# Performance work log

Measured on AMD Instinct MI355X. Metric: run time of the kernel, lower is better.

## Reference

```python
import jax, jax.numpy as jnp
import numpy as np

ALPHA = 0.2  # LeakyReLU negative slope

def setup_inputs() -> dict:
    key = jax.random.key(0)
    k1, k2, k3, k4 = jax.random.split(key, 4)
    B, N, IN_C, OUT_C = 4, 4096, 64, 64
    features = jax.random.normal(k1, (B, N, IN_C), dtype=jnp.float32)
    adj = jax.random.uniform(k2, (B, N, N), dtype=jnp.float32)  # unused by the module's math
    # xavier_normal approximations
    W = jax.random.normal(k3, (IN_C, OUT_C), dtype=jnp.float32) * np.sqrt(2.0 / (IN_C + OUT_C))
    a = jax.random.normal(k4, (2 * OUT_C, 1), dtype=jnp.float32) * np.sqrt(2.0 / (2 * OUT_C + 1))
    return {"features": features, "adj": adj, "W": W, "a": a}

def reference(features, adj, W, a):
    # h: [B, N, F]
    h = jnp.matmul(features, W)
    out_c = W.shape[1]
    a1 = a[:out_c, 0]   # [F]
    a2 = a[out_c:, 0]   # [F]
    # e[b,i,j] = leakyrelu(h_i . a1 + h_j . a2)  (decomposed; avoids O(N^2*2F) concat)
    s1 = jnp.einsum('bnf,f->bn', h, a1)  # [B, N]
    s2 = jnp.einsum('bnf,f->bn', h, a2)  # [B, N]
    e = s1[:, :, None] + s2[:, None, :]  # [B, N, N]
    e = jnp.where(e >= 0, e, ALPHA * e)  # leaky relu
    attention = jax.nn.softmax(e, axis=2)  # note: adj is NOT used (faithful to source)
    h_prime = jnp.matmul(attention, h)  # [B, N, F]
    return h_prime
```

## Files before the change

kernel.cpp:

```cpp
#include <hip/hip_runtime.h>
#include <hip/hip_bf16.h>
#include <cmath>

#define LRALPHA 0.2f

namespace {
constexpr int BB = 4;
constexpr int NN = 4096;
constexpr int ROWS = BB * NN;
}

typedef __attribute__((ext_vector_type(8))) short bf16x8;
typedef __attribute__((ext_vector_type(4))) float f32x4;

static __device__ inline short f2bf(float x) {
  __hip_bfloat16 t = __float2bfloat16(x);
  return *reinterpret_cast<short*>(&t);
}
static __device__ inline float bf2f(short x) {
  __hip_bfloat16 t = *reinterpret_cast<__hip_bfloat16*>(&x);
  return __bfloat162float(t);
}
static __device__ inline unsigned int packRNE(float a, float b) {
  unsigned int ua = __float_as_uint(a), ub = __float_as_uint(b);
  unsigned int ra = ua + 0x7FFFu + ((ua >> 16) & 1u);
  unsigned int rb = ub + 0x7FFFu + ((ub >> 16) & 1u);
  return (ra >> 16) | (rb & 0xFFFF0000u);
}

__global__ __launch_bounds__(256) void k_hcvt(
    const float* __restrict__ feat, const float* __restrict__ W,
    const float* __restrict__ a,
    unsigned short* __restrict__ hTh, unsigned short* __restrict__ hTl,
    float* __restrict__ s1g, float* __restrict__ s2g) {
  __shared__ float tile[64][65];
  const int lane = threadIdx.x & 63;
  const int wave = threadIdx.x >> 6;
  const int row0 = blockIdx.x * 64;

  float wreg[64];
#pragma unroll
  for (int k = 0; k < 64; ++k) wreg[k] = W[k * 64 + lane];
  const float a1 = a[lane], a2 = a[64 + lane];

  for (int r = 0; r < 16; ++r) {
    const int row = row0 + wave * 16 + r;
    const float4* f4 = (const float4*)(feat + (size_t)row * 64);
    float hv = 0.f;
#pragma unroll
    for (int kk = 0; kk < 16; ++kk) {
      float4 f = f4[kk];
      hv = fmaf(f.x, wreg[4 * kk + 0], hv);
      hv = fmaf(f.y, wreg[4 * kk + 1], hv);
      hv = fmaf(f.z, wreg[4 * kk + 2], hv);
      hv = fmaf(f.w, wreg[4 * kk + 3], hv);
    }
    tile[wave * 16 + r][lane] = hv;
    float p1 = hv * a1, p2 = hv * a2;
#pragma unroll
    for (int off = 32; off; off >>= 1) {
      p1 += __shfl_xor(p1, off, 64);
      p2 += __shfl_xor(p2, off, 64);
    }
    if (lane == 0) { s1g[row] = p1; s2g[row] = p2; }
  }
  __syncthreads();

  const int b = row0 >> 12;
  const int n0 = row0 & (NN - 1);
#pragma unroll
  for (int cc = 0; cc < 16; ++cc) {
    int ch = cc * 4 + wave;
    float v = tile[lane][ch];
    short hi = f2bf(v);
    short lo = f2bf(v - bf2f(hi));
    size_t idx = ((size_t)(b * 64 + ch) << 12) + n0 + lane;
    hTh[idx] = (unsigned short)hi;
    hTl[idx] = (unsigned short)lo;
  }
}

__global__ void k_maxs2(const float* __restrict__ s2g, float* __restrict__ maxs2) {
  __shared__ float red[256];
  int b = blockIdx.x;
  float m = -1e30f;
  for (int j = threadIdx.x; j < NN; j += 256) m = fmaxf(m, s2g[b * NN + j]);
  red[threadIdx.x] = m;
  __syncthreads();
  for (int off = 128; off; off >>= 1) {
    if ((int)threadIdx.x < off) red[threadIdx.x] = fmaxf(red[threadIdx.x], red[threadIdx.x + off]);
    __syncthreads();
  }
  if (threadIdx.x == 0) maxs2[b] = red[0];
}

__global__ void k_prep(const float* __restrict__ s1g, const float* __restrict__ s2g,
                       const float* __restrict__ maxs2,
                       float* __restrict__ Ag, float* __restrict__ Apg,
                       float* __restrict__ Tg,
                       float* __restrict__ Bv, float* __restrict__ Bpv) {
  int row = blockIdx.x * 256 + threadIdx.x;
  int b = row >> 12;
  float s1 = s1g[row], s2 = s2g[row];
  float t = s1 + maxs2[b];
  float m = t >= 0.f ? t : LRALPHA * t;
  Ag[row]  = expf(s1 - m);
  Apg[row] = expf(LRALPHA * s1 - m);
  Tg[row]  = expf(-s1);
  Bv[row]  = expf(s2);
  Bpv[row] = expf(LRALPHA * s2);
}

__global__ __launch_bounds__(512, 4) void k_attn(
    const unsigned short* __restrict__ hTh, const unsigned short* __restrict__ hTl,
    const float* __restrict__ Ag, const float* __restrict__ Apg,
    const float* __restrict__ Tg,
    const float* __restrict__ Bv, const float* __restrict__ Bpv,
    float* __restrict__ out) {
  __shared__ float slab[4][32][65];
  __shared__ float l_lds[4][32];

  const int wave = threadIdx.x >> 6;
  const int lane = threadIdx.x & 63;
  const int m = lane & 15;
  const int quad = lane >> 4;
  const int row0 = blockIdx.x * 32;
  const int b = row0 >> 12;
  const int i0 = row0 + m, i1 = row0 + 16 + m;

  const float Ar0 = Ag[i0], Ap0 = Apg[i0], T0 = Tg[i0];
  const float Ar1 = Ag[i1], Ap1 = Apg[i1], T1 = Tg[i1];

  f32x4 acc00 = {0,0,0,0}, acc01 = {0,0,0,0}, acc02 = {0,0,0,0}, acc03 = {0,0,0,0};
  f32x4 acc10 = {0,0,0,0}, acc11 = {0,0,0,0}, acc12 = {0,0,0,0}, acc13 = {0,0,0,0};
  f32x4 lacc0 = {0,0,0,0}, lacc1 = {0,0,0,0};

  bf16x8 ones;
#pragma unroll
  for (int e = 0; e < 8; ++e) ones[e] = (short)0x3F80;

  const int j0 = wave * (NN / 8) + quad * 8;
  const float* Bq  = Bv  + (b << 12) + j0;
  const float* Bpq = Bpv + (b << 12) + j0;
  const unsigned short* hp = hTh + ((size_t)(b * 64 + m) << 12) + j0;
  const unsigned short* lp = hTl + ((size_t)(b * 64 + m) << 12) + j0;
  constexpr size_t CH16 = (size_t)16 << 12;

  for (int it = 0; it < NN / 8 / 32; ++it) {
    float4 bA = *(const float4*)(Bq);
    float4 bB = *(const float4*)(Bq + 4);
    float4 pA = *(const float4*)(Bpq);
    float4 pB = *(const float4*)(Bpq + 4);
    float bvv[8] = {bA.x, bA.y, bA.z, bA.w, bB.x, bB.y, bB.z, bB.w};
    float pvv[8] = {pA.x, pA.y, pA.z, pA.w, pB.x, pB.y, pB.z, pB.w};

    float w0v[8], w1v[8];
#pragma unroll
    for (int e = 0; e < 8; ++e) {
      float Bj = bvv[e], Bpj = pvv[e];
      w0v[e] = (Bj >= T0) ? (Ar0 * Bj) : (Ap0 * Bpj);
      w1v[e] = (Bj >= T1) ? (Ar1 * Bj) : (Ap1 * Bpj);
    }
    union { bf16x8 v; unsigned int u[4]; } af0u, af1u;
#pragma unroll
    for (int p = 0; p < 4; ++p) {
      af0u.u[p] = packRNE(w0v[2 * p], w0v[2 * p + 1]);
      af1u.u[p] = packRNE(w1v[2 * p], w1v[2 * p + 1]);
    }
    bf16x8 af0 = af0u.v, af1 = af1u.v;

    bf16x8 hh0 = *(const bf16x8*)(hp);
    bf16x8 hh1 = *(const bf16x8*)(hp + CH16);
    bf16x8 hh2 = *(const bf16x8*)(hp + 2 * CH16);
    bf16x8 hh3 = *(const bf16x8*)(hp + 3 * CH16);
    bf16x8 hl0 = *(const bf16x8*)(lp);
    bf16x8 hl1 = *(const bf16x8*)(lp + CH16);
    bf16x8 hl2 = *(const bf16x8*)(lp + 2 * CH16);
    bf16x8 hl3 = *(const bf16x8*)(lp + 3 * CH16);

    lacc0 = __builtin_amdgcn_mfma_f32_16x16x32_bf16(af0, ones, lacc0, 0, 0, 0);
    lacc1 = __builtin_amdgcn_mfma_f32_16x16x32_bf16(af1, ones, lacc1, 0, 0, 0);
    acc00 = __builtin_amdgcn_mfma_f32_16x16x32_bf16(af0, hh0, acc00, 0, 0, 0);
    acc00 = __builtin_amdgcn_mfma_f32_16x16x32_bf16(af0, hl0, acc00, 0, 0, 0);
    acc01 = __builtin_amdgcn_mfma_f32_16x16x32_bf16(af0, hh1, acc01, 0, 0, 0);
    acc01 = __builtin_amdgcn_mfma_f32_16x16x32_bf16(af0, hl1, acc01, 0, 0, 0);
    acc02 = __builtin_amdgcn_mfma_f32_16x16x32_bf16(af0, hh2, acc02, 0, 0, 0);
    acc02 = __builtin_amdgcn_mfma_f32_16x16x32_bf16(af0, hl2, acc02, 0, 0, 0);
    acc03 = __builtin_amdgcn_mfma_f32_16x16x32_bf16(af0, hh3, acc03, 0, 0, 0);
    acc03 = __builtin_amdgcn_mfma_f32_16x16x32_bf16(af0, hl3, acc03, 0, 0, 0);
    acc10 = __builtin_amdgcn_mfma_f32_16x16x32_bf16(af1, hh0, acc10, 0, 0, 0);
    acc10 = __builtin_amdgcn_mfma_f32_16x16x32_bf16(af1, hl0, acc10, 0, 0, 0);
    acc11 = __builtin_amdgcn_mfma_f32_16x16x32_bf16(af1, hh1, acc11, 0, 0, 0);
    acc11 = __builtin_amdgcn_mfma_f32_16x16x32_bf16(af1, hl1, acc11, 0, 0, 0);
    acc12 = __builtin_amdgcn_mfma_f32_16x16x32_bf16(af1, hh2, acc12, 0, 0, 0);
    acc12 = __builtin_amdgcn_mfma_f32_16x16x32_bf16(af1, hl2, acc12, 0, 0, 0);
    acc13 = __builtin_amdgcn_mfma_f32_16x16x32_bf16(af1, hh3, acc13, 0, 0, 0);
    acc13 = __builtin_amdgcn_mfma_f32_16x16x32_bf16(af1, hl3, acc13, 0, 0, 0);

    Bq += 32; Bpq += 32; hp += 32; lp += 32;
  }

  const int sidx = wave & 3;
  if (wave < 4) {
#pragma unroll
    for (int reg = 0; reg < 4; ++reg) {
      int rl = quad * 4 + reg;
      slab[sidx][rl][m]      = acc00[reg];
      slab[sidx][rl][m + 16] = acc01[reg];
      slab[sidx][rl][m + 32] = acc02[reg];
      slab[sidx][rl][m + 48] = acc03[reg];
      slab[sidx][16 + rl][m]      = acc10[reg];
      slab[sidx][16 + rl][m + 16] = acc11[reg];
      slab[sidx][16 + rl][m + 32] = acc12[reg];
      slab[sidx][16 + rl][m + 48] = acc13[reg];
    }
    if (m == 0) {
#pragma unroll
      for (int reg = 0; reg < 4; ++reg) {
        l_lds[sidx][quad * 4 + reg]      = lacc0[reg];
        l_lds[sidx][16 + quad * 4 + reg] = lacc1[reg];
      }
    }
  }
  __syncthreads();
  if (wave >= 4) {
#pragma unroll
    for (int reg = 0; reg < 4; ++reg) {
      int rl = quad * 4 + reg;
      slab[sidx][rl][m]      += acc00[reg];
      slab[sidx][rl][m + 16] += acc01[reg];
      slab[sidx][rl][m + 32] += acc02[reg];
      slab[sidx][rl][m + 48] += acc03[reg];
      slab[sidx][16 + rl][m]      += acc10[reg];
      slab[sidx][16 + rl][m + 16] += acc11[reg];
      slab[sidx][16 + rl][m + 32] += acc12[reg];
      slab[sidx][16 + rl][m + 48] += acc13[reg];
    }
    if (m == 0) {
#pragma unroll
      for (int reg = 0; reg < 4; ++reg) {
        l_lds[sidx][quad * 4 + reg]      += lacc0[reg];
        l_lds[sidx][16 + quad * 4 + reg] += lacc1[reg];
      }
    }
  }
  __syncthreads();

#pragma unroll
  for (int k = 0; k < 4; ++k) {
    int f = threadIdx.x + 512 * k;
    int rl = f >> 6, c = f & 63;
    float s = slab[0][rl][c] + slab[1][rl][c] + slab[2][rl][c] + slab[3][rl][c];
    float L = l_lds[0][rl] + l_lds[1][rl] + l_lds[2][rl] + l_lds[3][rl];
    out[((size_t)(row0 + rl)) * 64 + c] = s / L;
  }
}


extern "C" void kernel_launch(void* const* d_in, const int* in_sizes, int n_in,
                              void* d_out, int out_size, void* d_ws, size_t ws_size,
                              hipStream_t stream) {
  const float* feat = (const float*)d_in[0];
  const float* W = (const float*)d_in[2];
  const float* a = (const float*)d_in[3];
  float* out = (float*)d_out;

  char* ws = (char*)d_ws;
  size_t off = 0;
  auto carve = [&](size_t bytes) -> char* {
    char* p = ws + off;
    off = (off + bytes + 255) & ~(size_t)255;
    return p;
  };
  unsigned short* hTh = (unsigned short*)carve((size_t)ROWS * 64 * sizeof(unsigned short));
  unsigned short* hTl = (unsigned short*)carve((size_t)ROWS * 64 * sizeof(unsigned short));
  float* s1g   = (float*)carve(ROWS * sizeof(float));
  float* s2g   = (float*)carve(ROWS * sizeof(float));
  float* Ag    = (float*)carve(ROWS * sizeof(float));
  float* Apg   = (float*)carve(ROWS * sizeof(float));
  float* Tg    = (float*)carve(ROWS * sizeof(float));
  float* Bv    = (float*)carve(ROWS * sizeof(float));
  float* Bpv   = (float*)carve(ROWS * sizeof(float));
  float* maxs2 = (float*)carve(16 * sizeof(float));

  k_hcvt<<<ROWS / 64, 256, 0, stream>>>(feat, W, a, hTh, hTl, s1g, s2g);
  k_maxs2<<<BB, 256, 0, stream>>>(s2g, maxs2);
  k_prep<<<ROWS / 256, 256, 0, stream>>>(s1g, s2g, maxs2, Ag, Apg, Tg, Bv, Bpv);
  k_attn<<<ROWS / 32, 512, 0, stream>>>(hTh, hTl, Ag, Apg, Tg, Bv, Bpv, out);
}
```

Before: 395.6 us.

## Fuse exp precompute into projection kernel, drop max shift, prefetch B values

```diff
diff --git a/kernel.cpp b/kernel.cpp
--- a/kernel.cpp
+++ b/kernel.cpp
@@ -32,7 +32,8 @@
     const float* __restrict__ feat, const float* __restrict__ W,
     const float* __restrict__ a,
     unsigned short* __restrict__ hTh, unsigned short* __restrict__ hTl,
-    float* __restrict__ s1g, float* __restrict__ s2g) {
+    float* __restrict__ Ag, float* __restrict__ Apg, float* __restrict__ Tg,
+    float* __restrict__ Bv, float* __restrict__ Bpv) {
   __shared__ float tile[64][65];
   const int lane = threadIdx.x & 63;
   const int wave = threadIdx.x >> 6;
@@ -62,7 +63,13 @@
       p1 += __shfl_xor(p1, off, 64);
       p2 += __shfl_xor(p2, off, 64);
     }
-    if (lane == 0) { s1g[row] = p1; s2g[row] = p2; }
+    if (lane == 0) {
+      Ag[row]  = expf(p1);
+      Apg[row] = expf(LRALPHA * p1);
+      Tg[row]  = expf(-p1);
+      Bv[row]  = expf(p2);
+      Bpv[row] = expf(LRALPHA * p2);
+    }
   }
   __syncthreads();
 
@@ -80,37 +87,6 @@
   }
 }
 
-__global__ void k_maxs2(const float* __restrict__ s2g, float* __restrict__ maxs2) {
-  __shared__ float red[256];
-  int b = blockIdx.x;
-  float m = -1e30f;
-  for (int j = threadIdx.x; j < NN; j += 256) m = fmaxf(m, s2g[b * NN + j]);
-  red[threadIdx.x] = m;
-  __syncthreads();
-  for (int off = 128; off; off >>= 1) {
-    if ((int)threadIdx.x < off) red[threadIdx.x] = fmaxf(red[threadIdx.x], red[threadIdx.x + off]);
-    __syncthreads();
-  }
-  if (threadIdx.x == 0) maxs2[b] = red[0];
-}
-
-__global__ void k_prep(const float* __restrict__ s1g, const float* __restrict__ s2g,
-                       const float* __restrict__ maxs2,
-                       float* __restrict__ Ag, float* __restrict__ Apg,
-                       float* __restrict__ Tg,
-                       float* __restrict__ Bv, float* __restrict__ Bpv) {
-  int row = blockIdx.x * 256 + threadIdx.x;
-  int b = row >> 12;
-  float s1 = s1g[row], s2 = s2g[row];
-  float t = s1 + maxs2[b];
-  float m = t >= 0.f ? t : LRALPHA * t;
-  Ag[row]  = expf(s1 - m);
-  Apg[row] = expf(LRALPHA * s1 - m);
-  Tg[row]  = expf(-s1);
-  Bv[row]  = expf(s2);
-  Bpv[row] = expf(LRALPHA * s2);
-}
-
 __global__ __launch_bounds__(512, 4) void k_attn(
     const unsigned short* __restrict__ hTh, const unsigned short* __restrict__ hTl,
     const float* __restrict__ Ag, const float* __restrict__ Apg,
@@ -140,34 +116,20 @@
   for (int e = 0; e < 8; ++e) ones[e] = (short)0x3F80;
 
   const int j0 = wave * (NN / 8) + quad * 8;
-  const float* Bq  = Bv  + (b << 12) + j0;
-  const float* Bpq = Bpv + (b << 12) + j0;
+  const float4* Bq4  = (const float4*)(Bv  + (b << 12) + j0);
+  const float4* Bpq4 = (const float4*)(Bpv + (b << 12) + j0);
   const unsigned short* hp = hTh + ((size_t)(b * 64 + m) << 12) + j0;
   const unsigned short* lp = hTl + ((size_t)(b * 64 + m) << 12) + j0;
   constexpr size_t CH16 = (size_t)16 << 12;
-
-  for (int it = 0; it < NN / 8 / 32; ++it) {
-    float4 bA = *(const float4*)(Bq);
-    float4 bB = *(const float4*)(Bq + 4);
-    float4 pA = *(const float4*)(Bpq);
-    float4 pB = *(const float4*)(Bpq + 4);
-    float bvv[8] = {bA.x, bA.y, bA.z, bA.w, bB.x, bB.y, bB.z, bB.w};
-    float pvv[8] = {pA.x, pA.y, pA.z, pA.w, pB.x, pB.y, pB.z, pB.w};
-
-    float w0v[8], w1v[8];
-#pragma unroll
-    for (int e = 0; e < 8; ++e) {
-      float Bj = bvv[e], Bpj = pvv[e];
-      w0v[e] = (Bj >= T0) ? (Ar0 * Bj) : (Ap0 * Bpj);
-      w1v[e] = (Bj >= T1) ? (Ar1 * Bj) : (Ap1 * Bpj);
-    }
-    union { bf16x8 v; unsigned int u[4]; } af0u, af1u;
-#pragma unroll
-    for (int p = 0; p < 4; ++p) {
-      af0u.u[p] = packRNE(w0v[2 * p], w0v[2 * p + 1]);
-      af1u.u[p] = packRNE(w1v[2 * p], w1v[2 * p + 1]);
-    }
-    bf16x8 af0 = af0u.v, af1 = af1u.v;
+  constexpr int ITERS = NN / 8 / 32;
+
+  float4 bA = Bq4[0], bB = Bq4[1];
+  float4 pA = Bpq4[0], pB = Bpq4[1];
+
+  for (int it = 0; it < ITERS; ++it) {
+    Bq4 += 8; Bpq4 += 8;
+    float4 nbA = Bq4[0], nbB = Bq4[1];
+    float4 npA = Bpq4[0], npB = Bpq4[1];
 
     bf16x8 hh0 = *(const bf16x8*)(hp);
     bf16x8 hh1 = *(const bf16x8*)(hp + CH16);
@@ -177,6 +139,24 @@
     bf16x8 hl1 = *(const bf16x8*)(lp + CH16);
     bf16x8 hl2 = *(const bf16x8*)(lp + 2 * CH16);
     bf16x8 hl3 = *(const bf16x8*)(lp + 3 * CH16);
+
+    float bvv[8] = {bA.x, bA.y, bA.z, bA.w, bB.x, bB.y, bB.z, bB.w};
+    float pvv[8] = {pA.x, pA.y, pA.z, pA.w, pB.x, pB.y, pB.z, pB.w};
+
+    float w0v[8], w1v[8];
+#pragma unroll
+    for (int e = 0; e < 8; ++e) {
+      float Bj = bvv[e], Bpj = pvv[e];
+      w0v[e] = (Bj >= T0) ? (Ar0 * Bj) : (Ap0 * Bpj);
+      w1v[e] = (Bj >= T1) ? (Ar1 * Bj) : (Ap1 * Bpj);
+    }
+    union { bf16x8 v; unsigned int u[4]; } af0u, af1u;
+#pragma unroll
+    for (int p = 0; p < 4; ++p) {
+      af0u.u[p] = packRNE(w0v[2 * p], w0v[2 * p + 1]);
+      af1u.u[p] = packRNE(w1v[2 * p], w1v[2 * p + 1]);
+    }
+    bf16x8 af0 = af0u.v, af1 = af1u.v;
 
     lacc0 = __builtin_amdgcn_mfma_f32_16x16x32_bf16(af0, ones, lacc0, 0, 0, 0);
     lacc1 = __builtin_amdgcn_mfma_f32_16x16x32_bf16(af1, ones, lacc1, 0, 0, 0);
@@ -197,7 +177,8 @@
     acc13 = __builtin_amdgcn_mfma_f32_16x16x32_bf16(af1, hh3, acc13, 0, 0, 0);
     acc13 = __builtin_amdgcn_mfma_f32_16x16x32_bf16(af1, hl3, acc13, 0, 0, 0);
 
-    Bq += 32; Bpq += 32; hp += 32; lp += 32;
+    hp += 32; lp += 32;
+    bA = nbA; bB = nbB; pA = npA; pB = npB;
   }
 
   const int sidx = wave & 3;
@@ -274,17 +255,12 @@
   };
   unsigned short* hTh = (unsigned short*)carve((size_t)ROWS * 64 * sizeof(unsigned short));
   unsigned short* hTl = (unsigned short*)carve((size_t)ROWS * 64 * sizeof(unsigned short));
-  float* s1g   = (float*)carve(ROWS * sizeof(float));
-  float* s2g   = (float*)carve(ROWS * sizeof(float));
   float* Ag    = (float*)carve(ROWS * sizeof(float));
   float* Apg   = (float*)carve(ROWS * sizeof(float));
   float* Tg    = (float*)carve(ROWS * sizeof(float));
-  float* Bv    = (float*)carve(ROWS * sizeof(float));
-  float* Bpv   = (float*)carve(ROWS * sizeof(float));
-  float* maxs2 = (float*)carve(16 * sizeof(float));
-
-  k_hcvt<<<ROWS / 64, 256, 0, stream>>>(feat, W, a, hTh, hTl, s1g, s2g);
-  k_maxs2<<<BB, 256, 0, stream>>>(s2g, maxs2);
-  k_prep<<<ROWS / 256, 256, 0, stream>>>(s1g, s2g, maxs2, Ag, Apg, Tg, Bv, Bpv);
+  float* Bv    = (float*)carve((ROWS + 64) * sizeof(float));
+  float* Bpv   = (float*)carve((ROWS + 64) * sizeof(float));
+
+  k_hcvt<<<ROWS / 64, 256, 0, stream>>>(feat, W, a, hTh, hTl, Ag, Apg, Tg, Bv, Bpv);
   k_attn<<<ROWS / 32, 512, 0, stream>>>(hTh, hTl, Ag, Apg, Tg, Bv, Bpv, out);
 }
```

Result: no change. 391.1 us (-1.1%).
